# Kernel optimization log

Measured on AMD Instinct MI355X. Metric: run time of the kernel, lower is better.

Reference implementation:

```python
import jax, jax.numpy as jnp
import numpy as np
import math

B, T, C = 1, 2048, 2048
H, KVH = 32, 8
D = C // H  # 64
EPS = 1e-5
ROPE_THETA = 10000.0


def rmsnorm(x, w):
    # RMSNorm over last axis (head_dim), matches flax RMSNorm applied per-head
    var = jnp.mean(jnp.square(x), axis=-1, keepdims=True)
    return x * jax.lax.rsqrt(var + EPS) * w


def apply_rope(x, cos, sin):
    # x: [B, T, h, D]; cos/sin: [T, D//2]
    xr = x.reshape(*x.shape[:-1], D // 2, 2)
    x0, x1 = xr[..., 0], xr[..., 1]
    c = cos.reshape(1, T, 1, D // 2)
    s = sin.reshape(1, T, 1, D // 2)
    o0 = x0 * c - x1 * s
    o1 = x0 * s + x1 * c
    return jnp.stack([o0, o1], axis=-1).reshape(x.shape)


def setup_inputs() -> dict:
    key = jax.random.key(0)
    ks = jax.random.split(key, 12)
    x = jax.random.normal(ks[0], (B, T, C), jnp.float32)
    # RoPE tables
    inv_freq = 1.0 / (ROPE_THETA ** (np.arange(0, D, 2, dtype=np.float32) / D))
    angles = np.arange(T, dtype=np.float32)[:, None] * inv_freq[None, :]  # [T, D//2]
    freqs_cos = jnp.asarray(np.cos(angles))
    freqs_sin = jnp.asarray(np.sin(angles))
    # causal additive mask [1,1,T,T]
    causal = np.triu(np.full((T, T), -1e9, dtype=np.float32), k=1)
    mask = jnp.asarray(causal)[None, None]
    sc = lambda f: 1.0 / math.sqrt(f)
    return {
        "x": x,
        "freqs_cos": freqs_cos,
        "freqs_sin": freqs_sin,
        "mask": mask,
        "wq_k": jax.random.normal(ks[1], (C, H * D), jnp.float32) * sc(C),
        "wq_b": jnp.zeros((H * D,), jnp.float32),
        "wk_k": jax.random.normal(ks[2], (C, KVH * D), jnp.float32) * sc(C),
        "wk_b": jnp.zeros((KVH * D,), jnp.float32),
        "wv_k": jax.random.normal(ks[3], (C, KVH * D), jnp.float32) * sc(C),
        "wv_b": jnp.zeros((KVH * D,), jnp.float32),
        "wo_k": jax.random.normal(ks[4], (H * D, C), jnp.float32) * sc(H * D),
        "wo_b": jnp.zeros((C,), jnp.float32),
        "qn_w": jnp.ones((D,), jnp.float32),
        "kn_w": jnp.ones((D,), jnp.float32),
    }


def reference(x, freqs_cos, freqs_sin, mask, wq_k, wq_b, wk_k, wk_b, wv_k, wv_b, wo_k, wo_b, qn_w, kn_w):
    q = (x @ wq_k + wq_b).reshape(B, T, H, D)
    k = (x @ wk_k + wk_b).reshape(B, T, KVH, D)
    v = (x @ wv_k + wv_b).reshape(B, T, KVH, D)
    # QK RMSNorm over head_dim
    q = rmsnorm(q, qn_w)
    k = rmsnorm(k, kn_w)
    # RoPE
    q = apply_rope(q, freqs_cos, freqs_sin)
    k = apply_rope(k, freqs_cos, freqs_sin)
    # GQA repeat kv heads
    rep = H // KVH
    k = jnp.repeat(k, rep, axis=2)
    v = jnp.repeat(v, rep, axis=2)
    # [B, H, T, D]
    q, k, v = (jnp.swapaxes(t, 1, 2) for t in (q, k, v))
    scale = 1.0 / math.sqrt(D)
    scores = jnp.einsum("bhqd,bhkd->bhqk", q, k) * scale + mask
    attn = jax.nn.softmax(scores, axis=-1)
    out = jnp.einsum("bhqk,bhkd->bhqd", attn, v)
    out = jnp.swapaxes(out, 1, 2).reshape(B, T, H * D)
    return out @ wo_k + wo_b
```

## Files before the change

### kernel.cpp

```cpp
#include <hip/hip_runtime.h>
#include <hip/hip_bf16.h>
#include <cstdint>

typedef unsigned short u16;
typedef __attribute__((ext_vector_type(8))) short short8;
typedef __attribute__((ext_vector_type(4))) float f32x4;

__device__ __forceinline__ u16 f2bf(float f) {
  union { float f; uint32_t u; } c; c.f = f;
  return (u16)((c.u + 0x7FFFu + ((c.u >> 16) & 1u)) >> 16);
}

__device__ __forceinline__ uint32_t pack_bf16x2(float a, float b) {
  union { __hip_bfloat162 h; uint32_t u; } c;
  c.h = __float22bfloat162_rn(make_float2(a, b));
  return c.u;
}

__global__ __launch_bounds__(256) void conv_bf16(const float* __restrict__ in,
                                                 u16* __restrict__ out, int n4) {
  int i = blockIdx.x * 256 + threadIdx.x;
  if (i >= n4) return;
  float4 v = ((const float4*)in)[i];
  ((ushort4*)out)[i] = make_ushort4(f2bf(v.x), f2bf(v.y), f2bf(v.z), f2bf(v.w));
}

__global__ __launch_bounds__(256) void transpose_all(const float* __restrict__ wq,
                                                     const float* __restrict__ wk,
                                                     const float* __restrict__ wv,
                                                     const float* __restrict__ wo,
                                                     u16* __restrict__ wqkvT,
                                                     u16* __restrict__ woT) {
  __shared__ float tile[64][65];
  const int K = 2048;
  int bx = blockIdx.x;
  const float* in; u16* out; int N, nx;
  if (bx < 32)      { in = wq; out = wqkvT;                          N = 2048; nx = bx; }
  else if (bx < 40) { in = wk; out = wqkvT + (size_t)2048 * 2048;    N = 512;  nx = bx - 32; }
  else if (bx < 48) { in = wv; out = wqkvT + (size_t)2560 * 2048;    N = 512;  nx = bx - 40; }
  else              { in = wo; out = woT;                            N = 2048; nx = bx - 48; }
  int n0 = nx * 64, k0 = blockIdx.y * 64;
  int t = threadIdx.x;
  int a = t & 63, b4 = t >> 6;
#pragma unroll
  for (int j = 0; j < 16; ++j) {
    int kk = j * 4 + b4;
    tile[kk][a] = in[(size_t)(k0 + kk) * N + n0 + a];
  }
  __syncthreads();
#pragma unroll
  for (int j = 0; j < 16; ++j) {
    int nn = j * 4 + b4;
    out[(size_t)(n0 + nn) * K + k0 + a] = f2bf(tile[a][nn]);
  }
}

__global__ __launch_bounds__(256, 3) void gemm_qkv(const u16* __restrict__ A,
                                                   const u16* __restrict__ Bt,
                                                   const float* __restrict__ wq_b,
                                                   const float* __restrict__ wk_b,
                                                   const float* __restrict__ wv_b,
                                                   const float* __restrict__ qn_w,
                                                   const float* __restrict__ kn_w,
                                                   const float* __restrict__ fc,
                                                   const float* __restrict__ fs,
                                                   u16* __restrict__ Qg,
                                                   u16* __restrict__ Kg,
                                                   u16* __restrict__ Vg) {
  const int K = 2048, nb = 24;
  __shared__ alignas(16) u16 As[2][64 * 64];
  __shared__ alignas(16) u16 Bs[2][128 * 64];
  int nwg = gridDim.x;
  int cpx = nwg >> 3;
  int bid = blockIdx.x;
  int swz = (bid & 7) * cpx + (bid >> 3);
  int m0 = (swz / nb) << 6;
  int tileN = swz % nb;
  int n0 = tileN << 7;
  int tid = threadIdx.x;
  int w = tid >> 6, lane = tid & 63;
  int wr = w >> 1, wc = w & 1;
  int fr = lane & 15, hi = lane >> 4;
  int sw = fr & 7;

  auto STAGE = [&](int buf, int kt) {
#pragma unroll
    for (int i = 0; i < 2; ++i) {
      int chunk = i * 256 + tid;
      int row = chunk >> 3, c = chunk & 7;
      const u16* ga = A + (size_t)(m0 + row) * K + kt + ((c ^ (row & 7)) << 3);
      u16* la = &As[buf][(size_t)(i * 256 + w * 64) * 8];
      __builtin_amdgcn_global_load_lds((const __attribute__((address_space(1))) void*)ga,
                                       (__attribute__((address_space(3))) void*)la, 16, 0, 0);
    }
#pragma unroll
    for (int i = 0; i < 4; ++i) {
      int chunk = i * 256 + tid;
      int row = chunk >> 3, c = chunk & 7;
      const u16* gb = Bt + (size_t)(n0 + row) * K + kt + ((c ^ (row & 7)) << 3);
      u16* lb = &Bs[buf][(size_t)(i * 256 + w * 64) * 8];
      __builtin_amdgcn_global_load_lds((const __attribute__((address_space(1))) void*)gb,
                                       (__attribute__((address_space(3))) void*)lb, 16, 0, 0);
    }
  };

  f32x4 acc[2][4] = {};
  STAGE(0, 0);
  __syncthreads();
  int cur = 0;
  int c0 = (hi ^ sw) << 3, c1 = ((4 + hi) ^ sw) << 3;
  for (int kt = 0; kt < K; kt += 64) {
    if (kt + 64 < K) STAGE(cur ^ 1, kt + 64);
    short8 af[2][2], bf[4][2];
#pragma unroll
    for (int m = 0; m < 2; ++m) {
      int rb = (wr * 32 + m * 16 + fr) * 64;
      af[m][0] = *(const short8*)&As[cur][rb + c0];
      af[m][1] = *(const short8*)&As[cur][rb + c1];
    }
#pragma unroll
    for (int n = 0; n < 4; ++n) {
      int rb = (wc * 64 + n * 16 + fr) * 64;
      bf[n][0] = *(const short8*)&Bs[cur][rb + c0];
      bf[n][1] = *(const short8*)&Bs[cur][rb + c1];
    }
#pragma unroll
    for (int m = 0; m < 2; ++m)
#pragma unroll
      for (int n = 0; n < 4; ++n) {
        acc[m][n] = __builtin_amdgcn_mfma_f32_16x16x32_bf16(af[m][0], bf[n][0], acc[m][n], 0, 0, 0);
        acc[m][n] = __builtin_amdgcn_mfma_f32_16x16x32_bf16(af[m][1], bf[n][1], acc[m][n], 0, 0, 0);
      }
    __syncthreads();
    cur ^= 1;
  }

  int fbase = n0 + wc * 64;
  const float* bias; const float* nw = qn_w; u16* outp;
  bool isV = false; float nscale = 1.0f;
  if (fbase < 2048)      { outp = Qg + (size_t)(fbase >> 6) * 2048 * 64;          bias = wq_b + fbase;          nw = qn_w; nscale = 0.18033688f; }
  else if (fbase < 2560) { outp = Kg + (size_t)((fbase - 2048) >> 6) * 2048 * 64; bias = wk_b + (fbase - 2048); nw = kn_w; }
  else                   { outp = Vg + (size_t)((fbase - 2560) >> 6) * 2048 * 64; bias = wv_b + (fbase - 2560); isV = true; }

  float bv[4], nwv[4];
#pragma unroll
  for (int n = 0; n < 4; ++n) {
    bv[n] = bias[n * 16 + fr];
    nwv[n] = isV ? 0.0f : nw[n * 16 + fr] * nscale;
  }
#pragma unroll
  for (int m = 0; m < 2; ++m) {
#pragma unroll
    for (int r = 0; r < 4; ++r) {
      int t = m0 + wr * 32 + m * 16 + hi * 4 + r;
      float v[4];
      float sq = 0.0f;
#pragma unroll
      for (int n = 0; n < 4; ++n) { v[n] = acc[m][n][r] + bv[n]; sq += v[n] * v[n]; }
      if (!isV) {
        sq += __shfl_xor(sq, 1); sq += __shfl_xor(sq, 2);
        sq += __shfl_xor(sq, 4); sq += __shfl_xor(sq, 8);
        float rr = rsqrtf(sq * (1.0f / 64.0f) + 1e-5f);
#pragma unroll
        for (int n = 0; n < 4; ++n) {
          float vn = v[n] * rr * nwv[n];
          float part = __shfl_xor(vn, 1);
          int dh = n * 16 + fr;
          float c = fc[t * 32 + (dh >> 1)];
          float s = fs[t * 32 + (dh >> 1)];
          v[n] = (dh & 1) ? (part * s + vn * c) : (vn * c - part * s);
        }
      }
#pragma unroll
      for (int n = 0; n < 4; ++n)
        outp[(size_t)t * 64 + n * 16 + fr] = f2bf(v[n]);
    }
  }
}

__global__ __launch_bounds__(256, 3) void gemm_bt(const u16* __restrict__ A,
                                                  const u16* __restrict__ Bt,
                                                  float* __restrict__ C,
                                                  const float* __restrict__ bias,
                                                  int M, int N, int K) {
  __shared__ alignas(16) u16 As[2][64 * 64];
  __shared__ alignas(16) u16 Bs[2][128 * 64];
  int nb = N >> 7;
  int nwg = gridDim.x;
  int cpx = nwg >> 3;
  int bid = blockIdx.x;
  int swz = (bid & 7) * cpx + (bid >> 3);
  int m0 = (swz / nb) << 6;
  int n0 = (swz % nb) << 7;
  int tid = threadIdx.x;
  int w = tid >> 6, lane = tid & 63;
  int wr = w >> 1, wc = w & 1;
  int fr = lane & 15, hi = lane >> 4;
  int sw = fr & 7;

  auto STAGE = [&](int buf, int kt) {
#pragma unroll
    for (int i = 0; i < 2; ++i) {
      int chunk = i * 256 + tid;
      int row = chunk >> 3, c = chunk & 7;
      const u16* ga = A + (size_t)(m0 + row) * K + kt + ((c ^ (row & 7)) << 3);
      u16* la = &As[buf][(size_t)(i * 256 + w * 64) * 8];
      __builtin_amdgcn_global_load_lds((const __attribute__((address_space(1))) void*)ga,
                                       (__attribute__((address_space(3))) void*)la, 16, 0, 0);
    }
#pragma unroll
    for (int i = 0; i < 4; ++i) {
      int chunk = i * 256 + tid;
      int row = chunk >> 3, c = chunk & 7;
      const u16* gb = Bt + (size_t)(n0 + row) * K + kt + ((c ^ (row & 7)) << 3);
      u16* lb = &Bs[buf][(size_t)(i * 256 + w * 64) * 8];
      __builtin_amdgcn_global_load_lds((const __attribute__((address_space(1))) void*)gb,
                                       (__attribute__((address_space(3))) void*)lb, 16, 0, 0);
    }
  };

  f32x4 acc[2][4] = {};
  STAGE(0, 0);
  __syncthreads();
  int cur = 0;
  int c0 = (hi ^ sw) << 3, c1 = ((4 + hi) ^ sw) << 3;
  for (int kt = 0; kt < K; kt += 64) {
    if (kt + 64 < K) STAGE(cur ^ 1, kt + 64);
    short8 af[2][2], bf[4][2];
#pragma unroll
    for (int m = 0; m < 2; ++m) {
      int rb = (wr * 32 + m * 16 + fr) * 64;
      af[m][0] = *(const short8*)&As[cur][rb + c0];
      af[m][1] = *(const short8*)&As[cur][rb + c1];
    }
#pragma unroll
    for (int n = 0; n < 4; ++n) {
      int rb = (wc * 64 + n * 16 + fr) * 64;
      bf[n][0] = *(const short8*)&Bs[cur][rb + c0];
      bf[n][1] = *(const short8*)&Bs[cur][rb + c1];
    }
#pragma unroll
    for (int m = 0; m < 2; ++m)
#pragma unroll
      for (int n = 0; n < 4; ++n) {
        acc[m][n] = __builtin_amdgcn_mfma_f32_16x16x32_bf16(af[m][0], bf[n][0], acc[m][n], 0, 0, 0);
        acc[m][n] = __builtin_amdgcn_mfma_f32_16x16x32_bf16(af[m][1], bf[n][1], acc[m][n], 0, 0, 0);
      }
    __syncthreads();
    cur ^= 1;
  }
#pragma unroll
  for (int m = 0; m < 2; ++m) {
#pragma unroll
    for (int n = 0; n < 4; ++n) {
      int gcol = n0 + wc * 64 + n * 16 + fr;
      float bvx = bias ? bias[gcol] : 0.0f;
#pragma unroll
      for (int r = 0; r < 4; ++r) {
        int grow = m0 + wr * 32 + m * 16 + hi * 4 + r;
        C[(size_t)grow * N + gcol] = acc[m][n][r] + bvx;
      }
    }
  }
}

__global__ __launch_bounds__(256, 3) void attn_kernel(const u16* __restrict__ Qg,
                                                      const u16* __restrict__ Kg,
                                                      const u16* __restrict__ Vg,
                                                      const float* __restrict__ qn_w,
                                                      const float* __restrict__ kn_w,
                                                      u16* __restrict__ att) {
  __shared__ alignas(16) u16 Ks[2][64 * 64];
  __shared__ alignas(16) u16 Vs[2][64 * 64];
  __shared__ alignas(16) uint32_t Ps[4][16 * 36];

  int bid = blockIdx.x;
  int grp = bid >> 8, idx = bid & 255;
  int q0 = idx >> 5, h = idx & 31;
  int qt = (grp == 0) ? q0 : (grp == 1) ? 15 - q0 : (grp == 2) ? 16 + q0 : 31 - q0;
  int kvh = h >> 2;

  int tid = threadIdx.x, w = tid >> 6, lane = tid & 63;
  int fr = lane & 15, hi = lane >> 4, fk = hi * 8;

  float ba = fabsf(qn_w[lane]), bb = fabsf(kn_w[lane]);
#pragma unroll
  for (int off = 32; off >= 1; off >>= 1) {
    ba = fmaxf(ba, __shfl_xor(ba, off));
    bb = fmaxf(bb, __shfl_xor(bb, off));
  }
  float mfix = 11.5416222f * ba * bb;

  const u16* qbase = Qg + ((size_t)h * 2048 + qt * 64 + w * 16 + fr) * 64;
  short8 qf0 = *(const short8*)(qbase + fk);
  short8 qf1 = *(const short8*)(qbase + 32 + fk);
  f32x4 o[4] = {};
  float lrow = 0.0f;

  int key0 = tid >> 3, c0 = tid & 7;
  int kp = tid & 31, dg = tid >> 5, d0v = dg * 8;
  const u16* Kbase = Kg + (size_t)kvh * 2048 * 64;
  const u16* Vbase = Vg + (size_t)kvh * 2048 * 64;

  short8 k0r, k1r, v0r, v1r;
  auto stage_load = [&](int kt2) {
    const u16* kb = Kbase + (size_t)kt2 * 64 * 64;
    k0r = *(const short8*)(kb + key0 * 64 + c0 * 8);
    k1r = *(const short8*)(kb + (32 + key0) * 64 + c0 * 8);
    const u16* vb = Vbase + (size_t)kt2 * 64 * 64 + (size_t)(2 * kp) * 64 + d0v;
    v0r = *(const short8*)vb;
    v1r = *(const short8*)(vb + 64);
  };
  auto stage_write = [&](int buf) {
    char* KsB = (char*)&Ks[buf][0];
    char* VsB = (char*)&Vs[buf][0];
    int offA = (key0 * 128 + c0 * 16) ^ ((key0 & 7) << 4);
    int offB = ((32 + key0) * 128 + c0 * 16) ^ ((key0 & 7) << 4);
    *(short8*)(KsB + offA) = k0r;
    *(short8*)(KsB + offB) = k1r;
#pragma unroll
    for (int j = 0; j < 8; ++j) {
      uint32_t pk = (uint32_t)(u16)v0r[j] | ((uint32_t)(u16)v1r[j] << 16);
      int d = d0v + j;
      int off = (d * 128 + kp * 4) ^ ((j & 7) << 4);
      *(uint32_t*)(VsB + off) = pk;
    }
  };

  stage_load(0);
  stage_write(0);
  __syncthreads();

  uint32_t* Pw = &Ps[w][0];
  int swzr = (fr & 7) << 4;
  int qrow = qt * 64 + w * 16 + fr;

  for (int kt = 0; kt <= qt; ++kt) {
    int buf = kt & 1;
    bool diag = (kt == qt);
    if (!diag) stage_load(kt + 1);
    const char* KsB = (const char*)&Ks[buf][0];
    const char* VsB = (const char*)&Vs[buf][0];
    f32x4 s4[4] = {};
    __builtin_amdgcn_s_setprio(1);
#pragma unroll
    for (int g = 0; g < 4; ++g) {
      int rb = (g * 16 + fr) * 128;
      short8 b0 = *(const short8*)(KsB + ((rb + hi * 16) ^ swzr));
      short8 b1 = *(const short8*)(KsB + ((rb + 64 + hi * 16) ^ swzr));
      s4[g] = __builtin_amdgcn_mfma_f32_16x16x32_bf16(b0, qf0, s4[g], 0, 0, 0);
      s4[g] = __builtin_amdgcn_mfma_f32_16x16x32_bf16(b1, qf1, s4[g], 0, 0, 0);
    }
    __builtin_amdgcn_s_setprio(0);
    if (diag) {
      int kbase = kt * 64 + hi * 4;
#pragma unroll
      for (int g = 0; g < 4; ++g)
#pragma unroll
        for (int r = 0; r < 4; ++r)
          if (kbase + g * 16 + r > qrow) s4[g][r] = -1e30f;
    }
#pragma unroll
    for (int g = 0; g < 4; ++g) {
      float p0 = exp2f(s4[g][0] - mfix);
      float p1 = exp2f(s4[g][1] - mfix);
      float p2 = exp2f(s4[g][2] - mfix);
      float p3 = exp2f(s4[g][3] - mfix);
      lrow += (p0 + p1) + (p2 + p3);
      uint2 pk = make_uint2(pack_bf16x2(p0, p1), pack_bf16x2(p2, p3));
      *(uint2*)&Pw[fr * 36 + g * 8 + hi * 2] = pk;
    }
    asm volatile("s_waitcnt lgkmcnt(0)" ::: "memory");
    short8 pa0 = *(const short8*)&Pw[fr * 36 + hi * 4];
    short8 pa1 = *(const short8*)&Pw[fr * 36 + 16 + hi * 4];
    __builtin_amdgcn_s_setprio(1);
#pragma unroll
    for (int g2 = 0; g2 < 4; ++g2) {
      int rb = (g2 * 16 + fr) * 128;
      short8 vb0 = *(const short8*)(VsB + ((rb + hi * 16) ^ swzr));
      short8 vb1 = *(const short8*)(VsB + ((rb + 64 + hi * 16) ^ swzr));
      o[g2] = __builtin_amdgcn_mfma_f32_16x16x32_bf16(pa0, vb0, o[g2], 0, 0, 0);
      o[g2] = __builtin_amdgcn_mfma_f32_16x16x32_bf16(pa1, vb1, o[g2], 0, 0, 0);
    }
    __builtin_amdgcn_s_setprio(0);
    if (!diag) stage_write(buf ^ 1);
    __syncthreads();
  }
  float rtot = lrow;
  rtot += __shfl_xor(rtot, 16);
  rtot += __shfl_xor(rtot, 32);
#pragma unroll
  for (int r = 0; r < 4; ++r) {
    float li = __shfl(rtot, hi * 4 + r);
    float inv = 1.0f / li;
    size_t rowoff = (size_t)(qt * 64 + w * 16 + hi * 4 + r) * 2048 + h * 64;
#pragma unroll
    for (int g2 = 0; g2 < 4; ++g2)
      att[rowoff + g2 * 16 + fr] = f2bf(o[g2][r] * inv);
  }
}

extern "C" void kernel_launch(void* const* d_in, const int* in_sizes, int n_in,
                              void* d_out, int out_size, void* d_ws, size_t ws_size,
                              hipStream_t stream) {
  const float* x    = (const float*)d_in[0];
  const float* fc   = (const float*)d_in[1];
  const float* fs   = (const float*)d_in[2];
  const float* wq   = (const float*)d_in[4];
  const float* wq_b = (const float*)d_in[5];
  const float* wk   = (const float*)d_in[6];
  const float* wk_b = (const float*)d_in[7];
  const float* wv   = (const float*)d_in[8];
  const float* wv_b = (const float*)d_in[9];
  const float* wo   = (const float*)d_in[10];
  const float* wo_b = (const float*)d_in[11];
  const float* qn   = (const float*)d_in[12];
  const float* kn   = (const float*)d_in[13];
  float* out = (float*)d_out;

  char* ws = (char*)d_ws;
  u16*  xb    = (u16*)(ws);
  u16*  wqkvT = (u16*)(ws + (size_t)(8  << 20));
  u16*  woT   = (u16*)(ws + (size_t)(20 << 20));
  u16*  Qg    = (u16*)(ws + (size_t)(52 << 20));
  u16*  Kg    = (u16*)(ws + (size_t)(60 << 20));
  u16*  Vg    = (u16*)(ws + (size_t)(62 << 20));
  u16*  att   = (u16*)(ws + (size_t)(64 << 20));

  conv_bf16<<<4096, 256, 0, stream>>>(x, xb, 1048576);
  transpose_all<<<dim3(80, 32), 256, 0, stream>>>(wq, wk, wv, wo, wqkvT, woT);
  gemm_qkv<<<32 * 24, 256, 0, stream>>>(xb, wqkvT, wq_b, wk_b, wv_b, qn, kn, fc, fs, Qg, Kg, Vg);
  attn_kernel<<<1024, 256, 0, stream>>>(Qg, Kg, Vg, qn, kn, att);
  gemm_bt<<<32 * 16, 256, 0, stream>>>(att, woT, out, wo_b, 2048, 2048, 2048);
}
```

Baseline: 134.5 us.

## Store V transposed and stage K/V via direct global-to-LDS loads; merge prep kernels

```diff
diff --git a/kernel.cpp b/kernel.cpp
--- a/kernel.cpp
+++ b/kernel.cpp
@@ -17,29 +17,30 @@
   return c.u;
 }
 
-__global__ __launch_bounds__(256) void conv_bf16(const float* __restrict__ in,
-                                                 u16* __restrict__ out, int n4) {
-  int i = blockIdx.x * 256 + threadIdx.x;
-  if (i >= n4) return;
-  float4 v = ((const float4*)in)[i];
-  ((ushort4*)out)[i] = make_ushort4(f2bf(v.x), f2bf(v.y), f2bf(v.z), f2bf(v.w));
-}
-
-__global__ __launch_bounds__(256) void transpose_all(const float* __restrict__ wq,
-                                                     const float* __restrict__ wk,
-                                                     const float* __restrict__ wv,
-                                                     const float* __restrict__ wo,
-                                                     u16* __restrict__ wqkvT,
-                                                     u16* __restrict__ woT) {
+__global__ __launch_bounds__(256) void prep_kernel(const float* __restrict__ x,
+                                                   u16* __restrict__ xb,
+                                                   const float* __restrict__ wq,
+                                                   const float* __restrict__ wk,
+                                                   const float* __restrict__ wv,
+                                                   const float* __restrict__ wo,
+                                                   u16* __restrict__ wqkvT,
+                                                   u16* __restrict__ woT) {
+  int id = blockIdx.x;
+  if (id >= 2560) {
+    int i = (id - 2560) * 256 + threadIdx.x;
+    float4 v = ((const float4*)x)[i];
+    ((ushort4*)xb)[i] = make_ushort4(f2bf(v.x), f2bf(v.y), f2bf(v.z), f2bf(v.w));
+    return;
+  }
   __shared__ float tile[64][65];
   const int K = 2048;
-  int bx = blockIdx.x;
+  int bx = id % 80, by = id / 80;
   const float* in; u16* out; int N, nx;
   if (bx < 32)      { in = wq; out = wqkvT;                          N = 2048; nx = bx; }
   else if (bx < 40) { in = wk; out = wqkvT + (size_t)2048 * 2048;    N = 512;  nx = bx - 32; }
   else if (bx < 48) { in = wv; out = wqkvT + (size_t)2560 * 2048;    N = 512;  nx = bx - 40; }
   else              { in = wo; out = woT;                            N = 2048; nx = bx - 48; }
-  int n0 = nx * 64, k0 = blockIdx.y * 64;
+  int n0 = nx * 64, k0 = by * 64;
   int t = threadIdx.x;
   int a = t & 63, b4 = t >> 6;
 #pragma unroll
@@ -66,7 +67,7 @@
                                                    const float* __restrict__ fs,
                                                    u16* __restrict__ Qg,
                                                    u16* __restrict__ Kg,
-                                                   u16* __restrict__ Vg) {
+                                                   u16* __restrict__ Vgt) {
   const int K = 2048, nb = 24;
   __shared__ alignas(16) u16 As[2][64 * 64];
   __shared__ alignas(16) u16 Bs[2][128 * 64];
@@ -75,8 +76,7 @@
   int bid = blockIdx.x;
   int swz = (bid & 7) * cpx + (bid >> 3);
   int m0 = (swz / nb) << 6;
-  int tileN = swz % nb;
-  int n0 = tileN << 7;
+  int n0 = (swz % nb) << 7;
   int tid = threadIdx.x;
   int w = tid >> 6, lane = tid & 63;
   int wr = w >> 1, wc = w & 1;
@@ -136,17 +136,34 @@
   }
 
   int fbase = n0 + wc * 64;
-  const float* bias; const float* nw = qn_w; u16* outp;
-  bool isV = false; float nscale = 1.0f;
-  if (fbase < 2048)      { outp = Qg + (size_t)(fbase >> 6) * 2048 * 64;          bias = wq_b + fbase;          nw = qn_w; nscale = 0.18033688f; }
-  else if (fbase < 2560) { outp = Kg + (size_t)((fbase - 2048) >> 6) * 2048 * 64; bias = wk_b + (fbase - 2048); nw = kn_w; }
-  else                   { outp = Vg + (size_t)((fbase - 2560) >> 6) * 2048 * 64; bias = wv_b + (fbase - 2560); isV = true; }
-
+  if (fbase >= 2560) {
+    const float* bias = wv_b + (fbase - 2560);
+    u16* vt = Vgt + (size_t)(fbase - 2560) * 2048;
+    float bv[4];
+#pragma unroll
+    for (int n = 0; n < 4; ++n) bv[n] = bias[n * 16 + fr];
+#pragma unroll
+    for (int m = 0; m < 2; ++m)
+#pragma unroll
+      for (int r = 0; r < 4; ++r) {
+        int t = m0 + wr * 32 + m * 16 + hi * 4 + r;
+#pragma unroll
+        for (int n = 0; n < 4; ++n)
+          vt[(size_t)(n * 16 + fr) * 2048 + t] = f2bf(acc[m][n][r] + bv[n]);
+      }
+    return;
+  }
+  bool isQ = (fbase < 2048);
+  const float* bias = isQ ? wq_b + fbase : wk_b + (fbase - 2048);
+  const float* nw   = isQ ? qn_w : kn_w;
+  float nscale      = isQ ? 0.18033688f : 1.0f;
+  u16* outp = isQ ? Qg + (size_t)(fbase >> 6) * 2048 * 64
+                  : Kg + (size_t)((fbase - 2048) >> 6) * 2048 * 64;
   float bv[4], nwv[4];
 #pragma unroll
   for (int n = 0; n < 4; ++n) {
     bv[n] = bias[n * 16 + fr];
-    nwv[n] = isV ? 0.0f : nw[n * 16 + fr] * nscale;
+    nwv[n] = nw[n * 16 + fr] * nscale;
   }
 #pragma unroll
   for (int m = 0; m < 2; ++m) {
@@ -157,19 +174,17 @@
       float sq = 0.0f;
 #pragma unroll
       for (int n = 0; n < 4; ++n) { v[n] = acc[m][n][r] + bv[n]; sq += v[n] * v[n]; }
-      if (!isV) {
-        sq += __shfl_xor(sq, 1); sq += __shfl_xor(sq, 2);
-        sq += __shfl_xor(sq, 4); sq += __shfl_xor(sq, 8);
-        float rr = rsqrtf(sq * (1.0f / 64.0f) + 1e-5f);
-#pragma unroll
-        for (int n = 0; n < 4; ++n) {
-          float vn = v[n] * rr * nwv[n];
-          float part = __shfl_xor(vn, 1);
-          int dh = n * 16 + fr;
-          float c = fc[t * 32 + (dh >> 1)];
-          float s = fs[t * 32 + (dh >> 1)];
-          v[n] = (dh & 1) ? (part * s + vn * c) : (vn * c - part * s);
-        }
+      sq += __shfl_xor(sq, 1); sq += __shfl_xor(sq, 2);
+      sq += __shfl_xor(sq, 4); sq += __shfl_xor(sq, 8);
+      float rr = rsqrtf(sq * (1.0f / 64.0f) + 1e-5f);
+#pragma unroll
+      for (int n = 0; n < 4; ++n) {
+        float vn = v[n] * rr * nwv[n];
+        float part = __shfl_xor(vn, 1);
+        int dh = n * 16 + fr;
+        float c = fc[t * 32 + (dh >> 1)];
+        float s = fs[t * 32 + (dh >> 1)];
+        v[n] = (dh & 1) ? (part * s + vn * c) : (vn * c - part * s);
       }
 #pragma unroll
       for (int n = 0; n < 4; ++n)
@@ -266,7 +281,7 @@
 
 __global__ __launch_bounds__(256, 3) void attn_kernel(const u16* __restrict__ Qg,
                                                       const u16* __restrict__ Kg,
-                                                      const u16* __restrict__ Vg,
+                                                      const u16* __restrict__ Vgt,
                                                       const float* __restrict__ qn_w,
                                                       const float* __restrict__ kn_w,
                                                       u16* __restrict__ att) {
@@ -297,38 +312,26 @@
   f32x4 o[4] = {};
   float lrow = 0.0f;
 
-  int key0 = tid >> 3, c0 = tid & 7;
-  int kp = tid & 31, dg = tid >> 5, d0v = dg * 8;
   const u16* Kbase = Kg + (size_t)kvh * 2048 * 64;
-  const u16* Vbase = Vg + (size_t)kvh * 2048 * 64;
-
-  short8 k0r, k1r, v0r, v1r;
-  auto stage_load = [&](int kt2) {
-    const u16* kb = Kbase + (size_t)kt2 * 64 * 64;
-    k0r = *(const short8*)(kb + key0 * 64 + c0 * 8);
-    k1r = *(const short8*)(kb + (32 + key0) * 64 + c0 * 8);
-    const u16* vb = Vbase + (size_t)kt2 * 64 * 64 + (size_t)(2 * kp) * 64 + d0v;
-    v0r = *(const short8*)vb;
-    v1r = *(const short8*)(vb + 64);
+  const u16* Vtbase = Vgt + (size_t)kvh * 64 * 2048;
+  int row0 = tid >> 3, cc = tid & 7;
+
+  auto stage = [&](int buf, int kt) {
+#pragma unroll
+    for (int i = 0; i < 2; ++i) {
+      int row = i * 32 + row0;
+      const u16* srcK = Kbase + ((size_t)(kt * 64 + row)) * 64 + ((cc ^ (row & 7)) << 3);
+      u16* dstK = &Ks[buf][(size_t)(i * 256 + w * 64) * 8];
+      __builtin_amdgcn_global_load_lds((const __attribute__((address_space(1))) void*)srcK,
+                                       (__attribute__((address_space(3))) void*)dstK, 16, 0, 0);
+      const u16* srcV = Vtbase + (size_t)row * 2048 + kt * 64 + ((cc ^ (row & 7)) << 3);
+      u16* dstV = &Vs[buf][(size_t)(i * 256 + w * 64) * 8];
+      __builtin_amdgcn_global_load_lds((const __attribute__((address_space(1))) void*)srcV,
+                                       (__attribute__((address_space(3))) void*)dstV, 16, 0, 0);
+    }
   };
-  auto stage_write = [&](int buf) {
-    char* KsB = (char*)&Ks[buf][0];
-    char* VsB = (char*)&Vs[buf][0];
-    int offA = (key0 * 128 + c0 * 16) ^ ((key0 & 7) << 4);
-    int offB = ((32 + key0) * 128 + c0 * 16) ^ ((key0 & 7) << 4);
-    *(short8*)(KsB + offA) = k0r;
-    *(short8*)(KsB + offB) = k1r;
-#pragma unroll
-    for (int j = 0; j < 8; ++j) {
-      uint32_t pk = (uint32_t)(u16)v0r[j] | ((uint32_t)(u16)v1r[j] << 16);
-      int d = d0v + j;
-      int off = (d * 128 + kp * 4) ^ ((j & 7) << 4);
-      *(uint32_t*)(VsB + off) = pk;
-    }
-  };
-
-  stage_load(0);
-  stage_write(0);
+
+  stage(0, 0);
   __syncthreads();
 
   uint32_t* Pw = &Ps[w][0];
@@ -338,7 +341,7 @@
   for (int kt = 0; kt <= qt; ++kt) {
     int buf = kt & 1;
     bool diag = (kt == qt);
-    if (!diag) stage_load(kt + 1);
+    if (!diag) stage(buf ^ 1, kt + 1);
     const char* KsB = (const char*)&Ks[buf][0];
     const char* VsB = (const char*)&Vs[buf][0];
     f32x4 s4[4] = {};
@@ -383,7 +386,6 @@
       o[g2] = __builtin_amdgcn_mfma_f32_16x16x32_bf16(pa1, vb1, o[g2], 0, 0, 0);
     }
     __builtin_amdgcn_s_setprio(0);
-    if (!diag) stage_write(buf ^ 1);
     __syncthreads();
   }
   float rtot = lrow;
@@ -424,12 +426,11 @@
   u16*  woT   = (u16*)(ws + (size_t)(20 << 20));
   u16*  Qg    = (u16*)(ws + (size_t)(52 << 20));
   u16*  Kg    = (u16*)(ws + (size_t)(60 << 20));
-  u16*  Vg    = (u16*)(ws + (size_t)(62 << 20));
+  u16*  Vgt   = (u16*)(ws + (size_t)(62 << 20));
   u16*  att   = (u16*)(ws + (size_t)(64 << 20));
 
-  conv_bf16<<<4096, 256, 0, stream>>>(x, xb, 1048576);
-  transpose_all<<<dim3(80, 32), 256, 0, stream>>>(wq, wk, wv, wo, wqkvT, woT);
-  gemm_qkv<<<32 * 24, 256, 0, stream>>>(xb, wqkvT, wq_b, wk_b, wv_b, qn, kn, fc, fs, Qg, Kg, Vg);
-  attn_kernel<<<1024, 256, 0, stream>>>(Qg, Kg, Vg, qn, kn, att);
+  prep_kernel<<<6656, 256, 0, stream>>>(x, xb, wq, wk, wv, wo, wqkvT, woT);
+  gemm_qkv<<<32 * 24, 256, 0, stream>>>(xb, wqkvT, wq_b, wk_b, wv_b, qn, kn, fc, fs, Qg, Kg, Vgt);
+  attn_kernel<<<1024, 256, 0, stream>>>(Qg, Kg, Vgt, qn, kn, att);
   gemm_bt<<<32 * 16, 256, 0, stream>>>(att, woT, out, wo_b, 2048, 2048, 2048);
 }
```

Result: no change. 134.0 us (-0.4%).
